# Performance work log

Hardware: AMD Instinct MI355X
Metric: run time of the kernel (lower is better)

## Reference

```python
import jax, jax.numpy as jnp
import numpy as np

N_NODES = 100000
EPS = 1e-12  # F.normalize eps


def _sage_conv(x, src, dst, deg, Wl, bl, Wr):
    # mean aggregation of neighbor (source) features at destination nodes
    agg = jax.ops.segment_sum(x[src], dst, num_segments=N_NODES)  # [N, F]
    agg = agg / jnp.maximum(deg, 1.0)[:, None]
    out = agg @ Wl + bl + x @ Wr  # lin_l(mean(x_j)) + lin_r(x_i)
    # normalize=True -> L2 row normalization
    norm = jnp.sqrt(jnp.sum(out * out, axis=-1, keepdims=True))
    return out / jnp.maximum(norm, EPS)


def setup_inputs() -> dict:
    key = jax.random.key(0)
    ks = jax.random.split(key, 10)
    F_IN, H, C = 14, 32, 2
    x = jax.random.normal(ks[0], (N_NODES, F_IN), dtype=jnp.float32)
    edge_index = jax.random.randint(ks[1], (2, 6400000), 0, N_NODES, dtype=jnp.int32)
    def glorot(k, shape):
        lim = float(np.sqrt(6.0 / (shape[0] + shape[1])))
        return jax.random.uniform(k, shape, jnp.float32, -lim, lim)
    return {
        "x": x,
        "edge_index": edge_index,
        "W1l": glorot(ks[2], (F_IN, H)), "b1": jnp.zeros((H,), jnp.float32),
        "W1r": glorot(ks[3], (F_IN, H)),
        "W2l": glorot(ks[4], (H, H)), "b2": jnp.zeros((H,), jnp.float32),
        "W2r": glorot(ks[5], (H, H)),
        "Wlin": glorot(ks[6], (H, C)), "blin": jnp.zeros((C,), jnp.float32),
    }


def reference(x, edge_index, W1l, b1, W1r, W2l, b2, W2r, Wlin, blin):
    src, dst = edge_index[0], edge_index[1]
    deg = jax.ops.segment_sum(jnp.ones_like(dst, dtype=x.dtype), dst,
                              num_segments=N_NODES)  # in-degree per node
    h = jax.nn.relu(_sage_conv(x, src, dst, deg, W1l, b1, W1r))
    # dropout p=0.2 is identity at inference
    h = jax.nn.relu(_sage_conv(h, src, dst, deg, W2l, b2, W2r))
    return h @ Wlin + blin  # [N, num_classes]
```

## Files before the change

### kernel.cpp

```cpp
#include <hip/hip_runtime.h>
#include <hip/hip_bf16.h>


#define CHA 16384
#define MAXB 512
#define CAPB 18432
#define NPB 128

static __device__ __forceinline__ unsigned short f2bf(float f) {
    unsigned u = __float_as_uint(f);
    unsigned r = (u + 0x7FFFu + ((u >> 16) & 1u)) >> 16;
    return (unsigned short)r;
}
#define BF_LO(u) __uint_as_float((u) << 16)
#define BF_HI(u) __uint_as_float((u) & 0xFFFF0000u)

__global__ void cvt_x_bf16(const float* __restrict__ x, unsigned short* __restrict__ xb,
                           int* __restrict__ bcursor, int N, int NB) {
    int idx = blockIdx.x * blockDim.x + threadIdx.x;
    if (idx < NB) bcursor[idx] = idx * CAPB;
    if (idx >= N * 16) return;
    int n = idx >> 4, f = idx & 15;
    float v = (f < 14) ? x[n * 14 + f] : 0.f;
    xb[idx] = f2bf(v);
}

__global__ __launch_bounds__(1024) void partitionA(
        const int* __restrict__ src, const int* __restrict__ dst,
        int* __restrict__ bcursor, unsigned* __restrict__ part, int E, int NB) {
    __shared__ unsigned pk[CHA];
    __shared__ int h[MAXB], lofs[MAXB], cur[MAXB], delta[MAXB], tmp[MAXB];
    int t = threadIdx.x;
    int base = blockIdx.x * CHA;
    int end = base + CHA; if (end > E) end = E;
    int cnt = end - base;

    int ed[16], es[16];
    for (int i = t; i < NB; i += 1024) h[i] = 0;
    __syncthreads();
    #pragma unroll
    for (int i = 0; i < 4; ++i) {
        int j = i * 4096 + t * 4;
        if (j + 4 <= cnt) {
            int4 d4 = *(const int4*)(dst + base + j);
            int4 s4 = *(const int4*)(src + base + j);
            ed[i*4+0] = d4.x; ed[i*4+1] = d4.y; ed[i*4+2] = d4.z; ed[i*4+3] = d4.w;
            es[i*4+0] = s4.x; es[i*4+1] = s4.y; es[i*4+2] = s4.z; es[i*4+3] = s4.w;
            atomicAdd(&h[d4.x >> 8], 1);
            atomicAdd(&h[d4.y >> 8], 1);
            atomicAdd(&h[d4.z >> 8], 1);
            atomicAdd(&h[d4.w >> 8], 1);
        } else {
            #pragma unroll
            for (int k = 0; k < 4; ++k) {
                if (j + k < cnt) {
                    ed[i*4+k] = dst[base + j + k];
                    es[i*4+k] = src[base + j + k];
                    atomicAdd(&h[ed[i*4+k] >> 8], 1);
                } else ed[i*4+k] = -1;
            }
        }
    }
    __syncthreads();
    int v = 0;
    if (t < MAXB) { v = (t < NB) ? h[t] : 0; tmp[t] = v; }
    __syncthreads();
    for (int off = 1; off < MAXB; off <<= 1) {
        int a = 0;
        if (t < MAXB && t >= off) a = tmp[t - off];
        __syncthreads();
        if (t < MAXB) tmp[t] += a;
        __syncthreads();
    }
    if (t < NB) {
        int excl = tmp[t] - v;
        lofs[t] = excl;
        cur[t] = excl;
        int g = v ? atomicAdd(&bcursor[t], v) : 0;
        delta[t] = g - excl;
    }
    __syncthreads();
    #pragma unroll
    for (int i = 0; i < 16; ++i) {
        int d = ed[i];
        if (d >= 0) {
            int b = d >> 8;
            int r = atomicAdd(&cur[b], 1);
            pk[r] = ((unsigned)(d & 255) << 24) | (unsigned)es[i];
        }
    }
    __syncthreads();
    int wid = t >> 6, lane = t & 63;
    for (int b = wid; b < NB; b += 16) {
        int s = lofs[b];
        int e2 = (b + 1 < NB) ? lofs[b + 1] : cnt;
        int dlt = delta[b];
        int lim = (b + 1) * CAPB;
        for (int k = s + lane; k < e2; k += 64) {
            int gidx = dlt + k;
            if (gidx < lim) part[gidx] = pk[k];
        }
    }
}

__global__ __launch_bounds__(1024) void partitionB_fused(
        const unsigned* __restrict__ part, const int* __restrict__ bcursor,
        const uint4* __restrict__ xb4, const float* __restrict__ x,
        const float* __restrict__ W1l, const float* __restrict__ b1,
        const float* __restrict__ W1r,
        int* __restrict__ deg, int* __restrict__ offs, int* __restrict__ nlo,
        int* __restrict__ sorted_src, float* __restrict__ hbuf,
        unsigned short* __restrict__ hb, int N, int HALF) {
    __shared__ int pk2[CAPB];
    __shared__ int hh[512], tmp[512], keyofs[512];
    __shared__ int lstart[256], ldeg[256];
    __shared__ float sagg[256 * 17];
    __shared__ float sx[256 * 14];
    __shared__ float swl[448], swr[448], sb1[32];
    int b = blockIdx.x;
    int t = threadIdx.x;
    int start = b * CAPB;
    int end = bcursor[b];
    if (end > start + CAPB) end = start + CAPB;
    int cnt = end - start;
    unsigned ce[18];
    if (t < 512) hh[t] = 0;
    if (t < 448) { swl[t] = W1l[t]; swr[t] = W1r[t]; }
    else if (t < 480) sb1[t - 448] = b1[t - 448];
    __syncthreads();
    #pragma unroll
    for (int i = 0; i < 18; ++i) {
        int idx = start + t + i * 1024;
        unsigned p = 0xFFFFFFFFu;
        if (idx < end) {
            p = part[idx];
            int key = (int)(p >> 24) * 2 + (((int)(p & 0xFFFFFFu) < HALF) ? 0 : 1);
            atomicAdd(&hh[key], 1);
        }
        ce[i] = p;
    }
    {
        int nnod = N - b * 256; if (nnod > 256) nnod = 256; if (nnod < 0) nnod = 0;
        const float* gx = x + (size_t)b * 256 * 14;
        for (int i = t; i < nnod * 14; i += 1024) sx[i] = gx[i];
    }
    __syncthreads();
    int v = (t < 512) ? hh[t] : 0;
    if (t < 512) tmp[t] = v;
    __syncthreads();
    for (int off = 1; off < 512; off <<= 1) {
        int a2 = (t < 512 && t >= off) ? tmp[t - off] : 0;
        __syncthreads();
        if (t < 512) tmp[t] += a2;
        __syncthreads();
    }
    if (t < 512) keyofs[t] = tmp[t] - v;
    __syncthreads();
    if (t < 256) {
        int lo = hh[2 * t];
        int d = lo + hh[2 * t + 1];
        int excl = keyofs[2 * t];
        lstart[t] = excl;
        ldeg[t] = d;
        int node = b * 256 + t;
        if (node < N) {
            deg[node] = d;
            offs[node] = start + excl;
            nlo[node] = lo;
        }
    }
    __syncthreads();
    #pragma unroll
    for (int i = 0; i < 18; ++i) {
        unsigned p = ce[i];
        if (p != 0xFFFFFFFFu) {
            int s = (int)(p & 0xFFFFFFu);
            int key = (int)(p >> 24) * 2 + ((s < HALF) ? 0 : 1);
            int r = atomicAdd(&keyofs[key], 1);
            pk2[r] = s;
        }
    }
    __syncthreads();
    for (int i = t; i < cnt; i += 1024)
        sorted_src[start + i] = pk2[i];

    int node = t >> 2, sub = t & 3, ep = sub >> 1, half = sub & 1;
    int js = lstart[node], d = ldeg[node];
    int je = js + d;
    float a[8] = {0,0,0,0,0,0,0,0};
    int j = js + ep;
    for (; j + 6 < je; j += 8) {
        int s0 = pk2[j], s1 = pk2[j+2], s2 = pk2[j+4], s3 = pk2[j+6];
        uint4 u0 = xb4[s0*2+half], u1 = xb4[s1*2+half], u2 = xb4[s2*2+half], u3 = xb4[s3*2+half];
        a[0] += BF_LO(u0.x)+BF_LO(u1.x)+BF_LO(u2.x)+BF_LO(u3.x);
        a[1] += BF_HI(u0.x)+BF_HI(u1.x)+BF_HI(u2.x)+BF_HI(u3.x);
        a[2] += BF_LO(u0.y)+BF_LO(u1.y)+BF_LO(u2.y)+BF_LO(u3.y);
        a[3] += BF_HI(u0.y)+BF_HI(u1.y)+BF_HI(u2.y)+BF_HI(u3.y);
        a[4] += BF_LO(u0.z)+BF_LO(u1.z)+BF_LO(u2.z)+BF_LO(u3.z);
        a[5] += BF_HI(u0.z)+BF_HI(u1.z)+BF_HI(u2.z)+BF_HI(u3.z);
        a[6] += BF_LO(u0.w)+BF_LO(u1.w)+BF_LO(u2.w)+BF_LO(u3.w);
        a[7] += BF_HI(u0.w)+BF_HI(u1.w)+BF_HI(u2.w)+BF_HI(u3.w);
    }
    for (; j < je; j += 2) {
        uint4 u0 = xb4[pk2[j]*2+half];
        a[0] += BF_LO(u0.x); a[1] += BF_HI(u0.x);
        a[2] += BF_LO(u0.y); a[3] += BF_HI(u0.y);
        a[4] += BF_LO(u0.z); a[5] += BF_HI(u0.z);
        a[6] += BF_LO(u0.w); a[7] += BF_HI(u0.w);
    }
    #pragma unroll
    for (int i = 0; i < 8; ++i) a[i] += __shfl_xor(a[i], 2);
    if (ep == 0) {
        #pragma unroll
        for (int i = 0; i < 8; ++i) sagg[node * 17 + half * 8 + i] = a[i];
    }
    __syncthreads();

    float inv = 1.0f / ((d > 0) ? (float)d : 1.0f);
    float acc[8];
    #pragma unroll
    for (int i = 0; i < 8; ++i) acc[i] = sb1[sub * 8 + i];
    #pragma unroll
    for (int k = 0; k < 14; ++k) {
        float ag = sagg[node * 17 + k] * inv;
        float xv = sx[node * 14 + k];
        const float4* wl4 = (const float4*)&swl[k * 32 + sub * 8];
        const float4* wr4 = (const float4*)&swr[k * 32 + sub * 8];
        float4 wla = wl4[0], wlb = wl4[1], wra = wr4[0], wrb = wr4[1];
        acc[0] += ag * wla.x + xv * wra.x;
        acc[1] += ag * wla.y + xv * wra.y;
        acc[2] += ag * wla.z + xv * wra.z;
        acc[3] += ag * wla.w + xv * wra.w;
        acc[4] += ag * wlb.x + xv * wrb.x;
        acc[5] += ag * wlb.y + xv * wrb.y;
        acc[6] += ag * wlb.z + xv * wrb.z;
        acc[7] += ag * wlb.w + xv * wrb.w;
    }
    float ss = 0.f;
    #pragma unroll
    for (int i = 0; i < 8; ++i) ss += acc[i] * acc[i];
    ss += __shfl_xor(ss, 1); ss += __shfl_xor(ss, 2);
    float invn = 1.f / fmaxf(sqrtf(ss), 1e-12f);
    int gnode = b * 256 + node;
    if (gnode < N) {
        float hv[8];
        #pragma unroll
        for (int i = 0; i < 8; ++i) hv[i] = fmaxf(acc[i] * invn, 0.f);
        float4* ho = (float4*)(hbuf + (size_t)gnode * 32 + sub * 8);
        ho[0] = make_float4(hv[0], hv[1], hv[2], hv[3]);
        ho[1] = make_float4(hv[4], hv[5], hv[6], hv[7]);
        uint4 pb;
        pb.x = (unsigned)f2bf(hv[0]) | ((unsigned)f2bf(hv[1]) << 16);
        pb.y = (unsigned)f2bf(hv[2]) | ((unsigned)f2bf(hv[3]) << 16);
        pb.z = (unsigned)f2bf(hv[4]) | ((unsigned)f2bf(hv[5]) << 16);
        pb.w = (unsigned)f2bf(hv[6]) | ((unsigned)f2bf(hv[7]) << 16);
        *(uint4*)(hb + (size_t)gnode * 32 + sub * 8) = pb;
    }
}

__global__ void gather32_p0(const uint4* __restrict__ hb, const int* __restrict__ sorted_src,
                            const int* __restrict__ offs, const int* __restrict__ nlo,
                            float4* __restrict__ agg2, int N) {
    int idx = blockIdx.x * blockDim.x + threadIdx.x;
    int n = idx >> 2;
    if (n >= N) return;
    int q = idx & 3;
    int start = offs[n];
    int jend = nlo[n];
    float a0=0,a1=0,a2=0,a3=0,a4=0,a5=0,a6=0,a7=0;
    int j = 0;
    for (; j + 4 <= jend; j += 4) {
        int s0 = sorted_src[start + j + 0];
        int s1 = sorted_src[start + j + 1];
        int s2 = sorted_src[start + j + 2];
        int s3 = sorted_src[start + j + 3];
        uint4 u0 = hb[s0 * 4 + q];
        uint4 u1 = hb[s1 * 4 + q];
        uint4 u2 = hb[s2 * 4 + q];
        uint4 u3 = hb[s3 * 4 + q];
        a0 += BF_LO(u0.x) + BF_LO(u1.x) + BF_LO(u2.x) + BF_LO(u3.x);
        a1 += BF_HI(u0.x) + BF_HI(u1.x) + BF_HI(u2.x) + BF_HI(u3.x);
        a2 += BF_LO(u0.y) + BF_LO(u1.y) + BF_LO(u2.y) + BF_LO(u3.y);
        a3 += BF_HI(u0.y) + BF_HI(u1.y) + BF_HI(u2.y) + BF_HI(u3.y);
        a4 += BF_LO(u0.z) + BF_LO(u1.z) + BF_LO(u2.z) + BF_LO(u3.z);
        a5 += BF_HI(u0.z) + BF_HI(u1.z) + BF_HI(u2.z) + BF_HI(u3.z);
        a6 += BF_LO(u0.w) + BF_LO(u1.w) + BF_LO(u2.w) + BF_LO(u3.w);
        a7 += BF_HI(u0.w) + BF_HI(u1.w) + BF_HI(u2.w) + BF_HI(u3.w);
    }
    for (; j < jend; ++j) {
        uint4 u0 = hb[sorted_src[start + j] * 4 + q];
        a0 += BF_LO(u0.x); a1 += BF_HI(u0.x);
        a2 += BF_LO(u0.y); a3 += BF_HI(u0.y);
        a4 += BF_LO(u0.z); a5 += BF_HI(u0.z);
        a6 += BF_LO(u0.w); a7 += BF_HI(u0.w);
    }
    agg2[n * 8 + q * 2 + 0] = make_float4(a0, a1, a2, a3);
    agg2[n * 8 + q * 2 + 1] = make_float4(a4, a5, a6, a7);
}

__global__ void gather32_p1(const uint4* __restrict__ hb, const int* __restrict__ sorted_src,
                            const int* __restrict__ offs, const int* __restrict__ deg,
                            const int* __restrict__ nlo, float4* __restrict__ agg2, int N) {
    int idx = blockIdx.x * blockDim.x + threadIdx.x;
    int n = idx >> 2;
    if (n >= N) return;
    int q = idx & 3;
    int start = offs[n];
    int d = deg[n];
    int j = nlo[n];
    float a0=0,a1=0,a2=0,a3=0,a4=0,a5=0,a6=0,a7=0;
    for (; j + 4 <= d; j += 4) {
        int s0 = sorted_src[start + j + 0];
        int s1 = sorted_src[start + j + 1];
        int s2 = sorted_src[start + j + 2];
        int s3 = sorted_src[start + j + 3];
        uint4 u0 = hb[s0 * 4 + q];
        uint4 u1 = hb[s1 * 4 + q];
        uint4 u2 = hb[s2 * 4 + q];
        uint4 u3 = hb[s3 * 4 + q];
        a0 += BF_LO(u0.x) + BF_LO(u1.x) + BF_LO(u2.x) + BF_LO(u3.x);
        a1 += BF_HI(u0.x) + BF_HI(u1.x) + BF_HI(u2.x) + BF_HI(u3.x);
        a2 += BF_LO(u0.y) + BF_LO(u1.y) + BF_LO(u2.y) + BF_LO(u3.y);
        a3 += BF_HI(u0.y) + BF_HI(u1.y) + BF_HI(u2.y) + BF_HI(u3.y);
        a4 += BF_LO(u0.z) + BF_LO(u1.z) + BF_LO(u2.z) + BF_LO(u3.z);
        a5 += BF_HI(u0.z) + BF_HI(u1.z) + BF_HI(u2.z) + BF_HI(u3.z);
        a6 += BF_LO(u0.w) + BF_LO(u1.w) + BF_LO(u2.w) + BF_LO(u3.w);
        a7 += BF_HI(u0.w) + BF_HI(u1.w) + BF_HI(u2.w) + BF_HI(u3.w);
    }
    for (; j < d; ++j) {
        uint4 u0 = hb[sorted_src[start + j] * 4 + q];
        a0 += BF_LO(u0.x); a1 += BF_HI(u0.x);
        a2 += BF_LO(u0.y); a3 += BF_HI(u0.y);
        a4 += BF_LO(u0.z); a5 += BF_HI(u0.z);
        a6 += BF_LO(u0.w); a7 += BF_HI(u0.w);
    }
    float inv = 1.0f / ((d > 0) ? (float)d : 1.0f);
    float4 p0 = agg2[n * 8 + q * 2 + 0];
    float4 p1 = agg2[n * 8 + q * 2 + 1];
    agg2[n * 8 + q * 2 + 0] = make_float4((p0.x + a0) * inv, (p0.y + a1) * inv,
                                          (p0.z + a2) * inv, (p0.w + a3) * inv);
    agg2[n * 8 + q * 2 + 1] = make_float4((p1.x + a4) * inv, (p1.y + a5) * inv,
                                          (p1.z + a6) * inv, (p1.w + a7) * inv);
}

__global__ __launch_bounds__(256) void dense2(
        const float* __restrict__ h, const float* __restrict__ agg2,
        const float* __restrict__ W2l, const float* __restrict__ b2,
        const float* __restrict__ W2r, const float* __restrict__ Wlin,
        const float* __restrict__ blin, float* __restrict__ out, int N) {
    __shared__ float sa[NPB * 33];
    __shared__ float sh2[NPB * 33];
    __shared__ float swl[32 * 32], swr[32 * 32], swo[64], sb[32], sbo[2];
    int t = threadIdx.x;
    int nb = blockIdx.x * NPB;
    int nn = N - nb; if (nn > NPB) nn = NPB;
    const float4* ga = (const float4*)(agg2 + (size_t)nb * 32);
    const float4* gh = (const float4*)(h + (size_t)nb * 32);
    for (int i = t; i < nn * 8; i += 256) {
        float4 v = ga[i];
        float* d = &sa[(i >> 3) * 33 + (i & 7) * 4];
        d[0] = v.x; d[1] = v.y; d[2] = v.z; d[3] = v.w;
        float4 w = gh[i];
        float* e = &sh2[(i >> 3) * 33 + (i & 7) * 4];
        e[0] = w.x; e[1] = w.y; e[2] = w.z; e[3] = w.w;
    }
    for (int i = t; i < 1024; i += 256) { swl[i] = W2l[i]; swr[i] = W2r[i]; }
    if (t < 64) swo[t] = Wlin[t];
    if (t < 32) sb[t] = b2[t];
    if (t < 2) sbo[t] = blin[t];
    __syncthreads();
    int q2 = t & 3;
    int p = t >> 2;
    int l0 = p * 2, l1 = l0 + 1;
    float acc0[8], acc1[8];
    #pragma unroll
    for (int j = 0; j < 8; ++j) { acc0[j] = sb[q2 * 8 + j]; acc1[j] = acc0[j]; }
    for (int k = 0; k < 32; ++k) {
        float a0 = sa[l0 * 33 + k],  a1 = sa[l1 * 33 + k];
        float h0 = sh2[l0 * 33 + k], h1 = sh2[l1 * 33 + k];
        const float4* wl4 = (const float4*)&swl[k * 32 + q2 * 8];
        const float4* wr4 = (const float4*)&swr[k * 32 + q2 * 8];
        float4 wla = wl4[0], wlb = wl4[1], wra = wr4[0], wrb = wr4[1];
        acc0[0] += a0 * wla.x + h0 * wra.x;  acc1[0] += a1 * wla.x + h1 * wra.x;
        acc0[1] += a0 * wla.y + h0 * wra.y;  acc1[1] += a1 * wla.y + h1 * wra.y;
        acc0[2] += a0 * wla.z + h0 * wra.z;  acc1[2] += a1 * wla.z + h1 * wra.z;
        acc0[3] += a0 * wla.w + h0 * wra.w;  acc1[3] += a1 * wla.w + h1 * wra.w;
        acc0[4] += a0 * wlb.x + h0 * wrb.x;  acc1[4] += a1 * wlb.x + h1 * wrb.x;
        acc0[5] += a0 * wlb.y + h0 * wrb.y;  acc1[5] += a1 * wlb.y + h1 * wrb.y;
        acc0[6] += a0 * wlb.z + h0 * wrb.z;  acc1[6] += a1 * wlb.z + h1 * wrb.z;
        acc0[7] += a0 * wlb.w + h0 * wrb.w;  acc1[7] += a1 * wlb.w + h1 * wrb.w;
    }
    float ss0 = 0.f, ss1 = 0.f;
    #pragma unroll
    for (int j = 0; j < 8; ++j) { ss0 += acc0[j] * acc0[j]; ss1 += acc1[j] * acc1[j]; }
    ss0 += __shfl_xor(ss0, 1); ss0 += __shfl_xor(ss0, 2);
    ss1 += __shfl_xor(ss1, 1); ss1 += __shfl_xor(ss1, 2);
    float inv0 = 1.f / fmaxf(sqrtf(ss0), 1e-12f);
    float inv1 = 1.f / fmaxf(sqrtf(ss1), 1e-12f);
    float o00 = 0.f, o01 = 0.f, o10 = 0.f, o11 = 0.f;
    #pragma unroll
    for (int j = 0; j < 8; ++j) {
        float hv0 = fmaxf(acc0[j] * inv0, 0.f);
        float hv1 = fmaxf(acc1[j] * inv1, 0.f);
        int kk = q2 * 8 + j;
        o00 += hv0 * swo[kk * 2 + 0];
        o01 += hv0 * swo[kk * 2 + 1];
        o10 += hv1 * swo[kk * 2 + 0];
        o11 += hv1 * swo[kk * 2 + 1];
    }
    o00 += __shfl_xor(o00, 1); o00 += __shfl_xor(o00, 2);
    o01 += __shfl_xor(o01, 1); o01 += __shfl_xor(o01, 2);
    o10 += __shfl_xor(o10, 1); o10 += __shfl_xor(o10, 2);
    o11 += __shfl_xor(o11, 1); o11 += __shfl_xor(o11, 2);
    if (q2 == 0) {
        int n0 = nb + l0, n1 = nb + l1;
        if (n0 < N) { out[n0 * 2 + 0] = o00 + sbo[0]; out[n0 * 2 + 1] = o01 + sbo[1]; }
        if (n1 < N) { out[n1 * 2 + 0] = o10 + sbo[0]; out[n1 * 2 + 1] = o11 + sbo[1]; }
    }
}

extern "C" void kernel_launch(void* const* d_in, const int* in_sizes, int n_in,
                              void* d_out, int out_size, void* d_ws, size_t ws_size,
                              hipStream_t stream) {
    const float* x    = (const float*)d_in[0];
    const int*   ei   = (const int*)d_in[1];
    const float* W1l  = (const float*)d_in[2];
    const float* b1   = (const float*)d_in[3];
    const float* W1r  = (const float*)d_in[4];
    const float* W2l  = (const float*)d_in[5];
    const float* b2   = (const float*)d_in[6];
    const float* W2r  = (const float*)d_in[7];
    const float* Wlin = (const float*)d_in[8];
    const float* blin = (const float*)d_in[9];
    float* out = (float*)d_out;

    const int N = in_sizes[0] / 14;
    const int E = in_sizes[1] / 2;
    const int* src = ei;
    const int* dst = ei + E;
    const int NB = (N + 255) / 256;
    const int HALF = N / 2;

    char* ws = (char*)d_ws;
    size_t off = 0;
    auto alloc = [&](size_t bytes) -> void* {
        void* p = ws + off;
        off = (off + bytes + 255) & ~(size_t)255;
        return p;
    };
    int*            bcursor    = (int*)alloc((size_t)NB * 4);
    unsigned*       part       = (unsigned*)alloc((size_t)NB * CAPB * 4);
    int*            sorted_src = (int*)alloc((size_t)NB * CAPB * 4);
    int*            deg        = (int*)alloc((size_t)N * 4);
    int*            offs       = (int*)alloc((size_t)N * 4);
    int*            nlo        = (int*)alloc((size_t)N * 4);
    unsigned short* xb         = (unsigned short*)alloc((size_t)N * 16 * 2);
    float*          hbuf       = (float*)alloc((size_t)N * 32 * 4);
    unsigned short* hb         = (unsigned short*)alloc((size_t)N * 32 * 2);
    float*          agg2       = (float*)part;
    (void)ws_size; (void)n_in; (void)out_size;

    cvt_x_bf16<<<(N * 16 + 255) / 256, 256, 0, stream>>>(x, xb, bcursor, N, NB);
    partitionA<<<(E + CHA - 1) / CHA, 1024, 0, stream>>>(src, dst, bcursor, part, E, NB);
    partitionB_fused<<<NB, 1024, 0, stream>>>(
        part, bcursor, (const uint4*)xb, x, W1l, b1, W1r,
        deg, offs, nlo, sorted_src, hbuf, hb, N, HALF);
    gather32_p0<<<(N * 4 + 255) / 256, 256, 0, stream>>>(
        (const uint4*)hb, sorted_src, offs, nlo, (float4*)agg2, N);
    gather32_p1<<<(N * 4 + 255) / 256, 256, 0, stream>>>(
        (const uint4*)hb, sorted_src, offs, deg, nlo, (float4*)agg2, N);
    dense2<<<(N + NPB - 1) / NPB, 256, 0, stream>>>(
        hbuf, agg2, W2l, b2, W2r, Wlin, blin, out, N);
}
```

Measured before the change: 273.2 us.

## Split partitionB_fused into two half-bucket blocks per destination bucket

Each 256-node destination bucket is now handled by two 1024-thread blocks, each taking 128 nodes. Every block scans all of the bucket's edges but keeps only those whose local destination falls in its half. LDS use per block roughly halves and there are twice as many blocks, which should raise occupancy and give each node 8 threads for the first-layer gather. The cost is that every edge in the partition buffer is read twice, and each half is capped at CAPH edges, so a very skewed bucket could overflow and be silently truncated.

```diff
diff --git a/kernel.cpp b/kernel.cpp
--- a/kernel.cpp
+++ b/kernel.cpp
@@ -5,6 +5,7 @@
 #define CHA 16384
 #define MAXB 512
 #define CAPB 18432
+#define CAPH 9728
 #define NPB 128
 
 static __device__ __forceinline__ unsigned short f2bf(float f) {
@@ -111,22 +112,24 @@
         int* __restrict__ deg, int* __restrict__ offs, int* __restrict__ nlo,
         int* __restrict__ sorted_src, float* __restrict__ hbuf,
         unsigned short* __restrict__ hb, int N, int HALF) {
-    __shared__ int pk2[CAPB];
-    __shared__ int hh[512], tmp[512], keyofs[512];
-    __shared__ int lstart[256], ldeg[256];
-    __shared__ float sagg[256 * 17];
-    __shared__ float sx[256 * 14];
+    __shared__ int pk2[CAPH];
+    __shared__ int hh[256], tmp[256], keyofs[256];
+    __shared__ int lstart[128], ldeg[128];
+    __shared__ float sagg[128 * 17];
+    __shared__ float sx[128 * 14];
     __shared__ float swl[448], swr[448], sb1[32];
-    int b = blockIdx.x;
+    __shared__ int sTot;
+    int b = blockIdx.x >> 1;
+    int halfId = blockIdx.x & 1;
     int t = threadIdx.x;
     int start = b * CAPB;
     int end = bcursor[b];
     if (end > start + CAPB) end = start + CAPB;
-    int cnt = end - start;
+    int rbase = blockIdx.x * CAPH;
     unsigned ce[18];
-    if (t < 512) hh[t] = 0;
-    if (t < 448) { swl[t] = W1l[t]; swr[t] = W1r[t]; }
-    else if (t < 480) sb1[t - 448] = b1[t - 448];
+    if (t < 256) hh[t] = 0;
+    if (t >= 512 && t < 960) { swl[t - 512] = W1l[t - 512]; swr[t - 512] = W1r[t - 512]; }
+    else if (t >= 960 && t < 992) sb1[t - 960] = b1[t - 960];
     __syncthreads();
     #pragma unroll
     for (int i = 0; i < 18; ++i) {
@@ -134,38 +137,43 @@
         unsigned p = 0xFFFFFFFFu;
         if (idx < end) {
             p = part[idx];
-            int key = (int)(p >> 24) * 2 + (((int)(p & 0xFFFFFFu) < HALF) ? 0 : 1);
-            atomicAdd(&hh[key], 1);
+            int dl = (int)(p >> 24);
+            if ((dl >> 7) == halfId) {
+                int key = (dl & 127) * 2 + (((int)(p & 0xFFFFFFu) < HALF) ? 0 : 1);
+                atomicAdd(&hh[key], 1);
+            } else p = 0xFFFFFFFFu;
         }
         ce[i] = p;
     }
     {
-        int nnod = N - b * 256; if (nnod > 256) nnod = 256; if (nnod < 0) nnod = 0;
-        const float* gx = x + (size_t)b * 256 * 14;
+        int nbase = b * 256 + halfId * 128;
+        int nnod = N - nbase; if (nnod > 128) nnod = 128; if (nnod < 0) nnod = 0;
+        const float* gx = x + (size_t)nbase * 14;
         for (int i = t; i < nnod * 14; i += 1024) sx[i] = gx[i];
     }
     __syncthreads();
-    int v = (t < 512) ? hh[t] : 0;
-    if (t < 512) tmp[t] = v;
-    __syncthreads();
-    for (int off = 1; off < 512; off <<= 1) {
-        int a2 = (t < 512 && t >= off) ? tmp[t - off] : 0;
+    int v = (t < 256) ? hh[t] : 0;
+    if (t < 256) tmp[t] = v;
+    __syncthreads();
+    for (int off = 1; off < 256; off <<= 1) {
+        int a2 = (t < 256 && t >= off) ? tmp[t - off] : 0;
         __syncthreads();
-        if (t < 512) tmp[t] += a2;
+        if (t < 256) tmp[t] += a2;
         __syncthreads();
     }
-    if (t < 512) keyofs[t] = tmp[t] - v;
-    __syncthreads();
-    if (t < 256) {
+    if (t < 256) keyofs[t] = tmp[t] - v;
+    if (t == 255) sTot = tmp[255];
+    __syncthreads();
+    if (t < 128) {
         int lo = hh[2 * t];
         int d = lo + hh[2 * t + 1];
         int excl = keyofs[2 * t];
         lstart[t] = excl;
         ldeg[t] = d;
-        int node = b * 256 + t;
+        int node = b * 256 + halfId * 128 + t;
         if (node < N) {
             deg[node] = d;
-            offs[node] = start + excl;
+            offs[node] = rbase + excl;
             nlo[node] = lo;
         }
     }
@@ -175,41 +183,46 @@
         unsigned p = ce[i];
         if (p != 0xFFFFFFFFu) {
             int s = (int)(p & 0xFFFFFFu);
-            int key = (int)(p >> 24) * 2 + ((s < HALF) ? 0 : 1);
+            int dl = (int)(p >> 24);
+            int key = (dl & 127) * 2 + ((s < HALF) ? 0 : 1);
             int r = atomicAdd(&keyofs[key], 1);
-            pk2[r] = s;
-        }
-    }
-    __syncthreads();
-    for (int i = t; i < cnt; i += 1024)
-        sorted_src[start + i] = pk2[i];
-
-    int node = t >> 2, sub = t & 3, ep = sub >> 1, half = sub & 1;
+            if (r < CAPH) pk2[r] = s;
+        }
+    }
+    __syncthreads();
+    int tot = sTot; if (tot > CAPH) tot = CAPH;
+    for (int i = t; i < tot; i += 1024)
+        sorted_src[rbase + i] = pk2[i];
+
+    int node = t >> 3, sub = t & 7, ep = sub >> 1, half = sub & 1;
     int js = lstart[node], d = ldeg[node];
     int je = js + d;
     float a[8] = {0,0,0,0,0,0,0,0};
     int j = js + ep;
-    for (; j + 6 < je; j += 8) {
-        int s0 = pk2[j], s1 = pk2[j+2], s2 = pk2[j+4], s3 = pk2[j+6];
-        uint4 u0 = xb4[s0*2+half], u1 = xb4[s1*2+half], u2 = xb4[s2*2+half], u3 = xb4[s3*2+half];
-        a[0] += BF_LO(u0.x)+BF_LO(u1.x)+BF_LO(u2.x)+BF_LO(u3.x);
-        a[1] += BF_HI(u0.x)+BF_HI(u1.x)+BF_HI(u2.x)+BF_HI(u3.x);
-        a[2] += BF_LO(u0.y)+BF_LO(u1.y)+BF_LO(u2.y)+BF_LO(u3.y);
-        a[3] += BF_HI(u0.y)+BF_HI(u1.y)+BF_HI(u2.y)+BF_HI(u3.y);
-        a[4] += BF_LO(u0.z)+BF_LO(u1.z)+BF_LO(u2.z)+BF_LO(u3.z);
-        a[5] += BF_HI(u0.z)+BF_HI(u1.z)+BF_HI(u2.z)+BF_HI(u3.z);
-        a[6] += BF_LO(u0.w)+BF_LO(u1.w)+BF_LO(u2.w)+BF_LO(u3.w);
-        a[7] += BF_HI(u0.w)+BF_HI(u1.w)+BF_HI(u2.w)+BF_HI(u3.w);
-    }
-    for (; j < je; j += 2) {
-        uint4 u0 = xb4[pk2[j]*2+half];
+    for (; j + 4 < je; j += 8) {
+        int s0 = pk2[j], s1 = pk2[j + 4];
+        uint4 u0 = xb4[s0 * 2 + half], u1 = xb4[s1 * 2 + half];
+        a[0] += BF_LO(u0.x) + BF_LO(u1.x);
+        a[1] += BF_HI(u0.x) + BF_HI(u1.x);
+        a[2] += BF_LO(u0.y) + BF_LO(u1.y);
+        a[3] += BF_HI(u0.y) + BF_HI(u1.y);
+        a[4] += BF_LO(u0.z) + BF_LO(u1.z);
+        a[5] += BF_HI(u0.z) + BF_HI(u1.z);
+        a[6] += BF_LO(u0.w) + BF_LO(u1.w);
+        a[7] += BF_HI(u0.w) + BF_HI(u1.w);
+    }
+    for (; j < je; j += 4) {
+        uint4 u0 = xb4[pk2[j] * 2 + half];
         a[0] += BF_LO(u0.x); a[1] += BF_HI(u0.x);
         a[2] += BF_LO(u0.y); a[3] += BF_HI(u0.y);
         a[4] += BF_LO(u0.z); a[5] += BF_HI(u0.z);
         a[6] += BF_LO(u0.w); a[7] += BF_HI(u0.w);
     }
     #pragma unroll
-    for (int i = 0; i < 8; ++i) a[i] += __shfl_xor(a[i], 2);
+    for (int i = 0; i < 8; ++i) {
+        a[i] += __shfl_xor(a[i], 2);
+        a[i] += __shfl_xor(a[i], 4);
+    }
     if (ep == 0) {
         #pragma unroll
         for (int i = 0; i < 8; ++i) sagg[node * 17 + half * 8 + i] = a[i];
@@ -217,44 +230,36 @@
     __syncthreads();
 
     float inv = 1.0f / ((d > 0) ? (float)d : 1.0f);
-    float acc[8];
-    #pragma unroll
-    for (int i = 0; i < 8; ++i) acc[i] = sb1[sub * 8 + i];
+    float acc[4];
+    #pragma unroll
+    for (int i = 0; i < 4; ++i) acc[i] = sb1[sub * 4 + i];
     #pragma unroll
     for (int k = 0; k < 14; ++k) {
         float ag = sagg[node * 17 + k] * inv;
         float xv = sx[node * 14 + k];
-        const float4* wl4 = (const float4*)&swl[k * 32 + sub * 8];
-        const float4* wr4 = (const float4*)&swr[k * 32 + sub * 8];
-        float4 wla = wl4[0], wlb = wl4[1], wra = wr4[0], wrb = wr4[1];
-        acc[0] += ag * wla.x + xv * wra.x;
-        acc[1] += ag * wla.y + xv * wra.y;
-        acc[2] += ag * wla.z + xv * wra.z;
-        acc[3] += ag * wla.w + xv * wra.w;
-        acc[4] += ag * wlb.x + xv * wrb.x;
-        acc[5] += ag * wlb.y + xv * wrb.y;
-        acc[6] += ag * wlb.z + xv * wrb.z;
-        acc[7] += ag * wlb.w + xv * wrb.w;
+        float4 wl = *(const float4*)&swl[k * 32 + sub * 4];
+        float4 wr = *(const float4*)&swr[k * 32 + sub * 4];
+        acc[0] += ag * wl.x + xv * wr.x;
+        acc[1] += ag * wl.y + xv * wr.y;
+        acc[2] += ag * wl.z + xv * wr.z;
+        acc[3] += ag * wl.w + xv * wr.w;
     }
     float ss = 0.f;
     #pragma unroll
-    for (int i = 0; i < 8; ++i) ss += acc[i] * acc[i];
-    ss += __shfl_xor(ss, 1); ss += __shfl_xor(ss, 2);
+    for (int i = 0; i < 4; ++i) ss += acc[i] * acc[i];
+    ss += __shfl_xor(ss, 1); ss += __shfl_xor(ss, 2); ss += __shfl_xor(ss, 4);
     float invn = 1.f / fmaxf(sqrtf(ss), 1e-12f);
-    int gnode = b * 256 + node;
+    int gnode = b * 256 + halfId * 128 + node;
     if (gnode < N) {
-        float hv[8];
+        float hv[4];
         #pragma unroll
-        for (int i = 0; i < 8; ++i) hv[i] = fmaxf(acc[i] * invn, 0.f);
-        float4* ho = (float4*)(hbuf + (size_t)gnode * 32 + sub * 8);
-        ho[0] = make_float4(hv[0], hv[1], hv[2], hv[3]);
-        ho[1] = make_float4(hv[4], hv[5], hv[6], hv[7]);
-        uint4 pb;
+        for (int i = 0; i < 4; ++i) hv[i] = fmaxf(acc[i] * invn, 0.f);
+        *(float4*)(hbuf + (size_t)gnode * 32 + sub * 4) =
+            make_float4(hv[0], hv[1], hv[2], hv[3]);
+        uint2 pb;
         pb.x = (unsigned)f2bf(hv[0]) | ((unsigned)f2bf(hv[1]) << 16);
         pb.y = (unsigned)f2bf(hv[2]) | ((unsigned)f2bf(hv[3]) << 16);
-        pb.z = (unsigned)f2bf(hv[4]) | ((unsigned)f2bf(hv[5]) << 16);
-        pb.w = (unsigned)f2bf(hv[6]) | ((unsigned)f2bf(hv[7]) << 16);
-        *(uint4*)(hb + (size_t)gnode * 32 + sub * 8) = pb;
+        *(uint2*)(hb + (size_t)gnode * 32 + sub * 4) = pb;
     }
 }
 
@@ -450,7 +455,7 @@
     };
     int*            bcursor    = (int*)alloc((size_t)NB * 4);
     unsigned*       part       = (unsigned*)alloc((size_t)NB * CAPB * 4);
-    int*            sorted_src = (int*)alloc((size_t)NB * CAPB * 4);
+    int*            sorted_src = (int*)alloc((size_t)NB * 2 * CAPH * 4);
     int*            deg        = (int*)alloc((size_t)N * 4);
     int*            offs       = (int*)alloc((size_t)N * 4);
     int*            nlo        = (int*)alloc((size_t)N * 4);
@@ -462,7 +467,7 @@
 
     cvt_x_bf16<<<(N * 16 + 255) / 256, 256, 0, stream>>>(x, xb, bcursor, N, NB);
     partitionA<<<(E + CHA - 1) / CHA, 1024, 0, stream>>>(src, dst, bcursor, part, E, NB);
-    partitionB_fused<<<NB, 1024, 0, stream>>>(
+    partitionB_fused<<<NB * 2, 1024, 0, stream>>>(
         part, bcursor, (const uint4*)xb, x, W1l, b1, W1r,
         deg, offs, nlo, sorted_src, hbuf, hb, N, HALF);
     gather32_p0<<<(N * 4 + 255) / 256, 256, 0, stream>>>(
```

Result: no change. 278.2 us (+1.8%).
